# Kernel optimization log

Hardware: AMD Instinct MI355X
Metric: run time of the kernel (lower is better)

The kernel has to match this reference:

```python
import jax, jax.numpy as jnp
import numpy as np

C_IN = 96          # spectral bands
D2 = 2 * C_IN      # d = 192 (inner dim)
D4 = 4 * D2        # 768 (4-directional scan channels)
N = 16             # SSM state size
DR = 6             # delta_rank = ceil(96/16)
B, H, W = 2, 96, 96  # H,W not in {8,16,32,64} -> s=1 path


def setup_inputs() -> dict:
    key = jax.random.key(0)
    ks = jax.random.split(key, 8)
    g = lambda k, shape, s: jax.random.normal(k, shape, jnp.float32) * s
    return {
        "x": jax.random.normal(ks[0], (B, C_IN, H, W), jnp.float32),
        "W_in": g(ks[1], (C_IN, 2 * D2), 0.05),          # in_proj (in,out)
        "b_in": jnp.zeros((2 * D2,), jnp.float32),
        "w_dw": g(ks[2], (D2, 1, 3, 3), 0.1),            # depthwise conv OIHW
        "b_dw": jnp.zeros((D2,), jnp.float32),
        "A_log": jnp.log(jnp.tile(jnp.arange(1.0, N + 1.0, dtype=jnp.float32), (D4, 1))),
        "Dp": jnp.ones((D4,), jnp.float32),
        "W_x": g(ks[3], (D4, DR + 2 * N), 0.05),         # x_proj, no bias
        "W_delta": g(ks[4], (DR, D4), 0.1),
        "b_delta": g(ks[5], (D4,), 0.1),
        "ln_g": jnp.ones((D2,), jnp.float32),
        "ln_b": jnp.zeros((D2,), jnp.float32),
        "W_out": g(ks[6], (D2, C_IN), 0.05),             # out_proj, no bias
    }


def _selective_scan(u, delta, A, Bm, Cm, Dv):
    # u, delta: [b,L,d4]; Bm, Cm: [b,L,n]; A: [d4,n]; Dv: [d4]
    b, L, d4 = u.shape
    n = A.shape[1]

    def step(h, inps):
        u_t, dt, B_t, C_t = inps                      # [b,d4],[b,d4],[b,n],[b,n]
        dA = jnp.exp(dt[:, :, None] * A)              # [b,d4,n]
        h = dA * h + (dt * u_t)[:, :, None] * B_t[:, None, :]
        y = jnp.einsum('bdn,bn->bd', h, C_t) + Dv * u_t
        return h, y

    h0 = jnp.zeros((b, d4, n), u.dtype)
    xs = (jnp.swapaxes(u, 0, 1), jnp.swapaxes(delta, 0, 1),
          jnp.swapaxes(Bm, 0, 1), jnp.swapaxes(Cm, 0, 1))
    _, ys = jax.lax.scan(step, h0, xs)                # ys: [L,b,d4]
    return jnp.swapaxes(ys, 0, 1)                     # [b,L,d4]


def reference(x, W_in, b_in, w_dw, b_dw, A_log, Dp, W_x, W_delta, b_delta, ln_g, ln_b, W_out):
    b, c, Hh, Ww = x.shape                            # s = 1 (H not in {8,16,32,64})
    d = W_in.shape[1] // 2
    # in_proj on channel-last, chunk into x / gate z
    xz = jnp.einsum('bchw,ce->bhwe', x, W_in) + b_in  # [b,h,w,2d]
    xx, z = jnp.split(xz, 2, axis=-1)
    # depthwise conv + silu
    xc = jnp.transpose(xx, (0, 3, 1, 2))              # [b,d,h,w]
    xc = jax.lax.conv_general_dilated(
        xc, w_dw, (1, 1), 'SAME', feature_group_count=d,
        dimension_numbers=('NCHW', 'OIHW', 'NCHW')) + b_dw[None, :, None, None]
    xc = jax.nn.silu(xc)
    # 4 directional flattenings (with s=1: x1==x2 row-major, x3==x4 reversed)
    L = Hh * Ww
    flat = xc.reshape(b, d, L)
    flipped = xc[:, :, ::-1, ::-1].reshape(b, d, L)
    xl = jnp.swapaxes(jnp.concatenate([flat, flat, flipped, flipped], axis=1), 1, 2)  # [b,L,4d]
    # SSM parameterization
    A = -jnp.exp(A_log)                               # [4d,n]
    x_dbl = xl @ W_x                                  # [b,L,dr+2n]
    dr, n = W_delta.shape[0], A.shape[1]
    dt_r = x_dbl[..., :dr]
    Bm = x_dbl[..., dr:dr + n]
    Cm = x_dbl[..., dr + n:]
    delta = jax.nn.softplus(dt_r @ W_delta + b_delta)  # [b,L,4d]
    y = _selective_scan(xl, delta, A, Bm, Cm, Dp)      # [b,L,4d]
    # merge 4 directions back to spatial
    y = jnp.transpose(y.reshape(b, L, 4, d), (0, 2, 3, 1))  # [b,4,d,L]
    y1 = y[:, 0].reshape(b, d, Hh, Ww)
    y2 = y[:, 1].reshape(b, d, Hh, Ww)
    y3 = y[:, 2].reshape(b, d, Hh, Ww)[:, :, ::-1, ::-1]
    y4 = y[:, 3].reshape(b, d, Hh, Ww)[:, :, ::-1, ::-1]
    yh = jnp.transpose(y1 + y2 + y3 + y4, (0, 2, 3, 1))  # [b,h,w,d]
    # LayerNorm over d
    mu = yh.mean(-1, keepdims=True)
    var = ((yh - mu) ** 2).mean(-1, keepdims=True)
    yn = (yh - mu) * jax.lax.rsqrt(var + 1e-5) * ln_g + ln_b
    out = (yn * jax.nn.silu(z)) @ W_out               # [b,h,w,c]
    return jnp.transpose(out, (0, 3, 1, 2))           # [b,c,h,w]
```

## Files before the change

### kernel.cpp

```cpp
#include <hip/hip_runtime.h>
#include <hip/hip_bf16.h>
#include <math.h>

#define CIN 96
#define D2 192
#define D4 768
#define LL 9216
#define NN 16
#define NCH 192
#define CLEN 48

typedef float v2f __attribute__((ext_vector_type(2)));

#define SZ_Y4SLOT (2u*2u*9216u*192u)
#define SZ_BL    (2u*9216u*192u)
#define SZ_XDBL  (2u*9216u*38u)
#define SZ_S     (2u*4u*192u*192u)
#define SZ_H     (2u*4u*192u*192u*16u)
#define F_Y4     0u
#define F_XX     0u
#define F_ZS     (F_Y4 + SZ_Y4SLOT)
#define F_XT     (F_ZS + SZ_BL)
#define F_XD0    (F_XT + SZ_BL)
#define F_XD1    (F_XD0 + SZ_XDBL)
#define F_XD2    (F_XD1 + SZ_XDBL)
#define F_XD3    (F_XD2 + SZ_XDBL)
#define F_SBUF   (F_XD3 + SZ_XDBL)
#define F_HBUF   (F_SBUF + SZ_S)
#define F_WCOMB  (F_HBUF + SZ_H)

__device__ __forceinline__ float silu_f(float z) {
    return z / (1.0f + __expf(-z));
}

__device__ __forceinline__ void pow_pairs(float e1, v2f p[8]) {
    float e2 = e1 * e1;
    v2f p01; p01.x = e1; p01.y = e2;
    v2f e2v; e2v.x = e2; e2v.y = e2;
    v2f e4v = e2v * e2v;
    v2f e8v = e4v * e4v;
    p[0] = p01;
    p[1] = p01 * e2v;
    p[2] = p01 * e4v;
    p[3] = p[1] * e4v;
    p[4] = p01 * e8v;
    p[5] = p[1] * e8v;
    p[6] = p[2] * e8v;
    p[7] = p[3] * e8v;
}

__global__ __launch_bounds__(256) void k0_foldw(
    const float* __restrict__ Wx, float* __restrict__ wcomb)
{
    int i = blockIdx.x * 256 + threadIdx.x;
    if (i >= 192 * 80) return;
    int d = i / 80, j = i % 80;
    float v = 0.f;
    if (j < 38) v = Wx[d * 38 + j] + Wx[(d + 192) * 38 + j];
    else if (j >= 40 && j < 78) {
        int jj = j - 40;
        v = Wx[(d + 384) * 38 + jj] + Wx[(d + 576) * 38 + jj];
    }
    wcomb[i] = v;
}

__global__ __launch_bounds__(256) void k1_inproj(
    const float* __restrict__ x, const float* __restrict__ Win,
    const float* __restrict__ bin, float* __restrict__ xx, float* __restrict__ zs)
{
    __shared__ float xs[96][68];
    __shared__ float wsm[96][68];
    int tid = threadIdx.x;
    int gl0 = blockIdx.x * 64;
    int b = gl0 / LL;
    int l0 = gl0 % LL;

    for (int i = tid; i < 96 * 64; i += 256) {
        int k = i >> 6, li = i & 63;
        xs[k][li] = x[(size_t)(b * 96 + k) * LL + l0 + li];
    }
    int lg = tid >> 4;
    int eg = tid & 15;
    for (int ech = 0; ech < 384; ech += 64) {
        __syncthreads();
        for (int i = tid; i < 96 * 64; i += 256) {
            int k = i >> 6, e = i & 63;
            wsm[k][e] = Win[k * 384 + ech + e];
        }
        __syncthreads();
        v2f acc2[4][2];
#pragma unroll
        for (int i = 0; i < 4; i++)
#pragma unroll
            for (int p = 0; p < 2; p++) { acc2[i][p].x = 0.f; acc2[i][p].y = 0.f; }
        for (int k = 0; k < 96; k++) {
            float4 xv = *(const float4*)&xs[k][lg * 4];
            float4 wv = *(const float4*)&wsm[k][eg * 4];
            v2f w0; w0.x = wv.x; w0.y = wv.y;
            v2f w1; w1.x = wv.z; w1.y = wv.w;
            float xa[4] = {xv.x, xv.y, xv.z, xv.w};
#pragma unroll
            for (int i = 0; i < 4; i++) {
                v2f xsp; xsp.x = xa[i]; xsp.y = xa[i];
                acc2[i][0] += xsp * w0;
                acc2[i][1] += xsp * w1;
            }
        }
        int e0 = ech + eg * 4;
        if (e0 < 192) {
#pragma unroll
            for (int j = 0; j < 4; j++) {
                int e = e0 + j;
                float bb = bin[e];
                float4 v = {acc2[0][j >> 1][j & 1] + bb, acc2[1][j >> 1][j & 1] + bb,
                            acc2[2][j >> 1][j & 1] + bb, acc2[3][j >> 1][j & 1] + bb};
                *(float4*)&xx[(size_t)(b * 192 + e) * LL + l0 + lg * 4] = v;
            }
        } else {
#pragma unroll
            for (int i = 0; i < 4; i++) {
                int l = l0 + lg * 4 + i;
                float4 v;
                v.x = silu_f(acc2[i][0][0] + bin[e0 + 0]);
                v.y = silu_f(acc2[i][0][1] + bin[e0 + 1]);
                v.z = silu_f(acc2[i][1][0] + bin[e0 + 2]);
                v.w = silu_f(acc2[i][1][1] + bin[e0 + 3]);
                *(float4*)&zs[((size_t)b * LL + l) * 192 + (e0 - 192)] = v;
            }
        }
    }
}

__global__ __launch_bounds__(192) void k2_conv(
    const float* __restrict__ xx, const float* __restrict__ wdw,
    const float* __restrict__ bdw, float* __restrict__ xt)
{
    __shared__ float tile[32][97];
    __shared__ float wsm[32][9];
    __shared__ float bs[32];
    int tid = threadIdx.x;
    int bid = blockIdx.x;
    int h = bid % 96;
    int r = bid / 96;
    int dg = r % 6;
    int b = r / 6;

    for (int i = tid; i < 288; i += 192) wsm[i / 9][i % 9] = wdw[(dg * 32 + i / 9) * 9 + (i % 9)];
    if (tid < 32) bs[tid] = bdw[dg * 32 + tid];
    __syncthreads();

    int w = tid % 96;
    int dhalf = tid / 96;
    for (int p = 0; p < 16; p++) {
        int dsub = 2 * p + dhalf;
        const float* base = xx + (size_t)(b * 192 + dg * 32 + dsub) * LL;
        float acc = bs[dsub];
#pragma unroll
        for (int kh = 0; kh < 3; kh++) {
            int hh = h + kh - 1;
            if (hh < 0 || hh >= 96) continue;
            const float* row = base + hh * 96;
#pragma unroll
            for (int kw = 0; kw < 3; kw++) {
                int ww = w + kw - 1;
                if (ww < 0 || ww >= 96) continue;
                acc += row[ww] * wsm[dsub][kh * 3 + kw];
            }
        }
        tile[dsub][w] = silu_f(acc);
    }
    __syncthreads();
    for (int i = tid; i < 768; i += 192) {
        int q = i & 7, ls = i >> 3;
        float4 v = {tile[q * 4 + 0][ls], tile[q * 4 + 1][ls], tile[q * 4 + 2][ls], tile[q * 4 + 3][ls]};
        *(float4*)&xt[((size_t)b * LL + h * 96 + ls) * 192 + dg * 32 + q * 4] = v;
    }
}

__global__ __launch_bounds__(320) void k3_xdbl(
    const float* __restrict__ xt, const float* __restrict__ wcomb,
    float* __restrict__ xa0, float* __restrict__ xa1,
    float* __restrict__ xb0, float* __restrict__ xb1)
{
    __shared__ float xs[16][68];
    __shared__ float wsh[16][80];
    int tid = threadIdx.x;
    int bid = blockIdx.x;
    int kh = bid & 1;
    int rt = (bid >> 1) % 144;
    int b = bid / 288;
    int r0 = rt * 64;
    int k0 = kh * 96;
    float* __restrict__ xa = kh ? xa1 : xa0;
    float* __restrict__ xb = kh ? xb1 : xb0;

    int rg = tid / 20;
    int cg = tid % 20;
    v2f acc[4][2];
#pragma unroll
    for (int i = 0; i < 4; i++)
#pragma unroll
        for (int p = 0; p < 2; p++) { acc[i][p].x = 0.f; acc[i][p].y = 0.f; }

    for (int kc = 0; kc < 96; kc += 16) {
        __syncthreads();
        if (tid < 256) {
            int row = tid >> 2, dq = tid & 3;
            float4 v = *(const float4*)&xt[((size_t)b * LL + r0 + row) * 192 + k0 + kc + dq * 4];
            xs[dq * 4 + 0][row] = v.x;
            xs[dq * 4 + 1][row] = v.y;
            xs[dq * 4 + 2][row] = v.z;
            xs[dq * 4 + 3][row] = v.w;
        }
        for (int i = tid; i < 16 * 80; i += 320) {
            int d = i / 80, j = i - d * 80;
            wsh[d][j] = wcomb[(k0 + kc + d) * 80 + j];
        }
        __syncthreads();
#pragma unroll
        for (int d = 0; d < 16; d++) {
            float4 xv = *(const float4*)&xs[d][rg * 4];
            float4 wv = *(const float4*)&wsh[d][cg * 4];
            v2f w01; w01.x = wv.x; w01.y = wv.y;
            v2f w23; w23.x = wv.z; w23.y = wv.w;
            float xr[4] = {xv.x, xv.y, xv.z, xv.w};
#pragma unroll
            for (int i = 0; i < 4; i++) {
                v2f xi; xi.x = xr[i]; xi.y = xr[i];
                acc[i][0] += xi * w01;
                acc[i][1] += xi * w23;
            }
        }
    }
    int c0 = cg * 4;
#pragma unroll
    for (int i = 0; i < 4; i++) {
        int la = r0 + rg * 4 + i;
#pragma unroll
        for (int j = 0; j < 4; j++) {
            int col = c0 + j;
            float v = acc[i][j >> 1][j & 1];
            if (col < 38) {
                xa[((size_t)b * LL + la) * 38 + col] = v;
            } else if (col >= 40 && col < 78) {
                int lb = LL - 1 - la;
                xb[((size_t)b * LL + lb) * 38 + (col - 40)] = v;
            }
        }
    }
}

__global__ __launch_bounds__(192, 4) void k4_pass1(
    const float* __restrict__ xt,
    const float* __restrict__ xa0, const float* __restrict__ xa1,
    const float* __restrict__ xb0, const float* __restrict__ xb1,
    const float* __restrict__ Wd, const float* __restrict__ bdl,
    const float* __restrict__ Alog,
    float* __restrict__ Sbuf, float* __restrict__ Hbuf)
{
    __shared__ float Bt[CLEN][16];
    __shared__ float Dt[CLEN][6];
    int tid = threadIdx.x;
    int bid = blockIdx.x;
    int k = bid % NCH;
    int r = bid / NCH;
    int dir = r & 3;
    int b = r >> 2;
    int l0 = k * CLEN;
    for (int i = tid; i < CLEN * 16; i += 192) {
        int t = i >> 4, n = i & 15;
        size_t rb = ((size_t)b * LL + l0 + t) * 38 + 6 + n;
        Bt[t][n] = (xa0[rb] + xa1[rb]) + (xb0[rb] + xb1[rb]);
    }
    for (int i = tid; i < CLEN * 6; i += 192) {
        int t = i / 6, rr = i - 6 * t;
        size_t rb = ((size_t)b * LL + l0 + t) * 38 + rr;
        Dt[t][rr] = (xa0[rb] + xa1[rb]) + (xb0[rb] + xb1[rb]);
    }
    __syncthreads();
    int c = tid;
    int d4 = dir * 192 + c;
    float a0 = -__expf(Alog[d4 * 16]);
    bool fast = true;
    for (int n = 1; n < 16; n++) {
        float an = -__expf(Alog[d4 * 16 + n]);
        float tgt = (n + 1) * a0;
        fast = fast && (fabsf(an - tgt) <= 1e-5f * fabsf(tgt));
    }
    float wd[6];
#pragma unroll
    for (int rr = 0; rr < 6; rr++) wd[rr] = Wd[rr * 768 + d4];
    float bde = bdl[d4];
    float S = 0.f;
    const float* xtp = xt + (size_t)b * LL * 192 + c;
    int bd = b * 4 + dir;
    size_t base = (((size_t)bd * NCH + k) * 192 + c) * 16;
    if (fast) {
        v2f h2[8];
#pragma unroll
        for (int n = 0; n < 8; n++) { h2[n].x = 0.f; h2[n].y = 0.f; }
        for (int t = 0; t < CLEN; t++) {
            float s = bde;
#pragma unroll
            for (int rr = 0; rr < 6; rr++) s += Dt[t][rr] * wd[rr];
            float dt = (s > 20.f) ? s : __logf(1.f + __expf(s));
            S += dt;
            int lp = (dir < 2) ? (l0 + t) : (LL - 1 - (l0 + t));
            float u = xtp[(size_t)lp * 192];
            float du = dt * u;
            float4 q0 = *(const float4*)&Bt[t][0];
            float4 q1 = *(const float4*)&Bt[t][4];
            float4 q2 = *(const float4*)&Bt[t][8];
            float4 q3 = *(const float4*)&Bt[t][12];
            v2f B2[8];
            B2[0].x = q0.x; B2[0].y = q0.y; B2[1].x = q0.z; B2[1].y = q0.w;
            B2[2].x = q1.x; B2[2].y = q1.y; B2[3].x = q1.z; B2[3].y = q1.w;
            B2[4].x = q2.x; B2[4].y = q2.y; B2[5].x = q2.z; B2[5].y = q2.w;
            B2[6].x = q3.x; B2[6].y = q3.y; B2[7].x = q3.z; B2[7].y = q3.w;
            v2f p2[8];
            pow_pairs(__expf(dt * a0), p2);
            v2f du2; du2.x = du; du2.y = du;
#pragma unroll
            for (int n = 0; n < 8; n++) h2[n] = p2[n] * h2[n] + du2 * B2[n];
        }
        v2f* hb = (v2f*)&Hbuf[base];
#pragma unroll
        for (int n = 0; n < 8; n++) hb[n] = h2[n];
    } else {
        float h[16];
#pragma unroll
        for (int n = 0; n < 16; n++) h[n] = 0.f;
        for (int t = 0; t < CLEN; t++) {
            float s = bde;
#pragma unroll
            for (int rr = 0; rr < 6; rr++) s += Dt[t][rr] * wd[rr];
            float dt = (s > 20.f) ? s : __logf(1.f + __expf(s));
            S += dt;
            int lp = (dir < 2) ? (l0 + t) : (LL - 1 - (l0 + t));
            float u = xtp[(size_t)lp * 192];
            float du = dt * u;
#pragma unroll
            for (int n = 0; n < 16; n++) {
                float e = __expf(dt * (-__expf(Alog[d4 * 16 + n])));
                h[n] = e * h[n] + du * Bt[t][n];
            }
        }
#pragma unroll
        for (int n = 0; n < 16; n++) Hbuf[base + n] = h[n];
    }
    Sbuf[((size_t)bd * NCH + k) * 192 + c] = S;
}

__global__ __launch_bounds__(256) void k4_pass2(
    const float* __restrict__ Sbuf, const float* __restrict__ Alog,
    float* __restrict__ Hbuf)
{
    int lane = blockIdx.x * 256 + threadIdx.x;
    int bd = lane / 3072;
    int cn = lane % 3072;
    int c = cn >> 4, n = cn & 15;
    int dir = bd & 3;
    float an = -__expf(Alog[(dir * 192 + c) * 16 + n]);
    float h = 0.f;
#pragma unroll 8
    for (int k = 0; k < NCH; k++) {
        size_t sidx = ((size_t)bd * NCH + k) * 192 + c;
        float S = Sbuf[sidx];
        size_t idx = sidx * 16 + n;
        float hl = Hbuf[idx];
        float P = __expf(an * S);
        Hbuf[idx] = h;
        h = P * h + hl;
    }
}

__global__ __launch_bounds__(192, 4) void k4_pass3(
    const float* __restrict__ xt,
    const float* __restrict__ xa0, const float* __restrict__ xa1,
    const float* __restrict__ xb0, const float* __restrict__ xb1,
    const float* __restrict__ Wd, const float* __restrict__ bdl,
    const float* __restrict__ Alog, const float* __restrict__ Dp,
    const float* __restrict__ Hbuf, __hip_bfloat16* __restrict__ y4)
{
    __shared__ float Bt[CLEN][16];
    __shared__ float Ct[CLEN][16];
    __shared__ float Dt[CLEN][6];
    int tid = threadIdx.x;
    int bid = blockIdx.x;
    int k = bid % NCH;
    int r = bid / NCH;
    int dir = r & 3;
    int b = r >> 2;
    int l0 = k * CLEN;
    for (int i = tid; i < CLEN * 16; i += 192) {
        int t = i >> 4, n = i & 15;
        size_t rb = ((size_t)b * LL + l0 + t) * 38;
        size_t r1 = rb + 6 + n, r2 = rb + 22 + n;
        Bt[t][n] = (xa0[r1] + xa1[r1]) + (xb0[r1] + xb1[r1]);
        Ct[t][n] = (xa0[r2] + xa1[r2]) + (xb0[r2] + xb1[r2]);
    }
    for (int i = tid; i < CLEN * 6; i += 192) {
        int t = i / 6, rr = i - 6 * t;
        size_t rb = ((size_t)b * LL + l0 + t) * 38 + rr;
        Dt[t][rr] = (xa0[rb] + xa1[rb]) + (xb0[rb] + xb1[rb]);
    }
    __syncthreads();
    int c = tid;
    int d4 = dir * 192 + c;
    float a0 = -__expf(Alog[d4 * 16]);
    bool fast = true;
    for (int n = 1; n < 16; n++) {
        float an = -__expf(Alog[d4 * 16 + n]);
        float tgt = (n + 1) * a0;
        fast = fast && (fabsf(an - tgt) <= 1e-5f * fabsf(tgt));
    }
    float wd[6];
#pragma unroll
    for (int rr = 0; rr < 6; rr++) wd[rr] = Wd[rr * 768 + d4];
    float bde = bdl[d4];
    float Dv = Dp[d4];
    int bd = b * 4 + dir;
    size_t base = (((size_t)bd * NCH + k) * 192 + c) * 16;
    const float* xtp = xt + (size_t)b * LL * 192 + c;
    __hip_bfloat16* yp = y4 + (size_t)bd * LL * 192 + c;
    if (fast) {
        v2f h2[8];
        const v2f* hb = (const v2f*)&Hbuf[base];
#pragma unroll
        for (int n = 0; n < 8; n++) h2[n] = hb[n];
        for (int t = 0; t < CLEN; t++) {
            float s = bde;
#pragma unroll
            for (int rr = 0; rr < 6; rr++) s += Dt[t][rr] * wd[rr];
            float dt = (s > 20.f) ? s : __logf(1.f + __expf(s));
            int lp = (dir < 2) ? (l0 + t) : (LL - 1 - (l0 + t));
            float u = xtp[(size_t)lp * 192];
            float du = dt * u;
            float4 q0 = *(const float4*)&Bt[t][0];
            float4 q1 = *(const float4*)&Bt[t][4];
            float4 q2 = *(const float4*)&Bt[t][8];
            float4 q3 = *(const float4*)&Bt[t][12];
            v2f B2[8];
            B2[0].x = q0.x; B2[0].y = q0.y; B2[1].x = q0.z; B2[1].y = q0.w;
            B2[2].x = q1.x; B2[2].y = q1.y; B2[3].x = q1.z; B2[3].y = q1.w;
            B2[4].x = q2.x; B2[4].y = q2.y; B2[5].x = q2.z; B2[5].y = q2.w;
            B2[6].x = q3.x; B2[6].y = q3.y; B2[7].x = q3.z; B2[7].y = q3.w;
            float4 r0 = *(const float4*)&Ct[t][0];
            float4 r1 = *(const float4*)&Ct[t][4];
            float4 r2 = *(const float4*)&Ct[t][8];
            float4 r3 = *(const float4*)&Ct[t][12];
            v2f C2[8];
            C2[0].x = r0.x; C2[0].y = r0.y; C2[1].x = r0.z; C2[1].y = r0.w;
            C2[2].x = r1.x; C2[2].y = r1.y; C2[3].x = r1.z; C2[3].y = r1.w;
            C2[4].x = r2.x; C2[4].y = r2.y; C2[5].x = r2.z; C2[5].y = r2.w;
            C2[6].x = r3.x; C2[6].y = r3.y; C2[7].x = r3.z; C2[7].y = r3.w;
            v2f p2[8];
            pow_pairs(__expf(dt * a0), p2);
            v2f du2; du2.x = du; du2.y = du;
            v2f ya; ya.x = 0.f; ya.y = 0.f;
            v2f yb; yb.x = 0.f; yb.y = 0.f;
#pragma unroll
            for (int n = 0; n < 8; n += 2) {
                h2[n] = p2[n] * h2[n] + du2 * B2[n];
                ya += h2[n] * C2[n];
                h2[n + 1] = p2[n + 1] * h2[n + 1] + du2 * B2[n + 1];
                yb += h2[n + 1] * C2[n + 1];
            }
            float yv = (ya.x + ya.y) + (yb.x + yb.y) + Dv * u;
            yp[(size_t)lp * 192] = __float2bfloat16(yv);
        }
    } else {
        float h[16];
#pragma unroll
        for (int n = 0; n < 16; n++) h[n] = Hbuf[base + n];
        for (int t = 0; t < CLEN; t++) {
            float s = bde;
#pragma unroll
            for (int rr = 0; rr < 6; rr++) s += Dt[t][rr] * wd[rr];
            float dt = (s > 20.f) ? s : __logf(1.f + __expf(s));
            int lp = (dir < 2) ? (l0 + t) : (LL - 1 - (l0 + t));
            float u = xtp[(size_t)lp * 192];
            float du = dt * u;
            float yv = Dv * u;
#pragma unroll
            for (int n = 0; n < 16; n++) {
                float e = __expf(dt * (-__expf(Alog[d4 * 16 + n])));
                h[n] = e * h[n] + du * Bt[t][n];
                yv += h[n] * Ct[t][n];
            }
            yp[(size_t)lp * 192] = __float2bfloat16(yv);
        }
    }
}

__global__ __launch_bounds__(256) void k5_out(
    const __hip_bfloat16* __restrict__ y4, const float* __restrict__ zs,
    const float* __restrict__ lng, const float* __restrict__ lnb,
    const float* __restrict__ Wout, float* __restrict__ out)
{
    __shared__ float acts[64][194];
    __shared__ float wsh[32][100];
    int tid = threadIdx.x;
    int wv = tid >> 6;
    int lane = tid & 63;
    int gl0 = blockIdx.x * 64;
    int b = gl0 / LL;
    int l0 = gl0 % LL;
    const size_t ds = (size_t)LL * 192;

    for (int i = 0; i < 16; i++) {
        int rrow = wv * 16 + i;
        int l = l0 + rrow;
        float yv[3], zv[3];
        float s1 = 0.f, s2 = 0.f;
#pragma unroll
        for (int kk = 0; kk < 3; kk++) {
            int c = lane + kk * 64;
            size_t off = ((size_t)(b * 4) * LL + l) * 192 + c;
            float y = __bfloat162float(y4[off]) + __bfloat162float(y4[off + ds])
                    + __bfloat162float(y4[off + 2 * ds]) + __bfloat162float(y4[off + 3 * ds]);
            yv[kk] = y;
            zv[kk] = zs[((size_t)b * LL + l) * 192 + c];
            s1 += y; s2 += y * y;
        }
#pragma unroll
        for (int o = 32; o; o >>= 1) {
            s1 += __shfl_xor(s1, o, 64);
            s2 += __shfl_xor(s2, o, 64);
        }
        float mean = s1 * (1.f / 192.f);
        float var = s2 * (1.f / 192.f) - mean * mean;
        float rs = rsqrtf(var + 1e-5f);
#pragma unroll
        for (int kk = 0; kk < 3; kk++) {
            int c = lane + kk * 64;
            float yn = (yv[kk] - mean) * rs * lng[c] + lnb[c];
            acts[rrow][c] = yn * zv[kk];
        }
    }

    int ty = tid >> 4;
    int tx = tid & 15;
    v2f o2[4][3];
#pragma unroll
    for (int i = 0; i < 4; i++)
#pragma unroll
        for (int p = 0; p < 3; p++) { o2[i][p].x = 0.f; o2[i][p].y = 0.f; }

    for (int kc = 0; kc < 192; kc += 32) {
        __syncthreads();
        for (int i = tid; i < 3072; i += 256)
            wsh[i / 96][i % 96] = Wout[(kc + i / 96) * 96 + i % 96];
        __syncthreads();
        for (int kk = 0; kk < 32; kk++) {
            float av[4];
#pragma unroll
            for (int i = 0; i < 4; i++) av[i] = acts[ty * 4 + i][kc + kk];
            const v2f* wp = (const v2f*)&wsh[kk][tx * 6];
            v2f w0 = wp[0], w1 = wp[1], w2 = wp[2];
#pragma unroll
            for (int i = 0; i < 4; i++) {
                v2f sp; sp.x = av[i]; sp.y = av[i];
                o2[i][0] += sp * w0;
                o2[i][1] += sp * w1;
                o2[i][2] += sp * w2;
            }
        }
    }
#pragma unroll
    for (int i = 0; i < 4; i++) {
        int l = l0 + ty * 4 + i;
#pragma unroll
        for (int j = 0; j < 6; j++) {
            int n = tx * 6 + j;
            out[((size_t)(b * 96) + n) * LL + l] = o2[i][j >> 1][j & 1];
        }
    }
}

extern "C" void kernel_launch(void* const* d_in, const int* in_sizes, int n_in,
                              void* d_out, int out_size, void* d_ws, size_t ws_size,
                              hipStream_t stream)
{
    const float* x    = (const float*)d_in[0];
    const float* Win  = (const float*)d_in[1];
    const float* bin  = (const float*)d_in[2];
    const float* wdw  = (const float*)d_in[3];
    const float* bdw  = (const float*)d_in[4];
    const float* Alog = (const float*)d_in[5];
    const float* Dp   = (const float*)d_in[6];
    const float* Wx   = (const float*)d_in[7];
    const float* Wd   = (const float*)d_in[8];
    const float* bdl  = (const float*)d_in[9];
    const float* lng  = (const float*)d_in[10];
    const float* lnb  = (const float*)d_in[11];
    const float* Wout = (const float*)d_in[12];
    float* out = (float*)d_out;

    float* ws    = (float*)d_ws;
    __hip_bfloat16* y4 = (__hip_bfloat16*)(ws + F_Y4);
    float* xx    = ws + F_XX;
    float* zs    = ws + F_ZS;
    float* xt    = ws + F_XT;
    float* xd0   = ws + F_XD0;
    float* xd1   = ws + F_XD1;
    float* xd2   = ws + F_XD2;
    float* xd3   = ws + F_XD3;
    float* Sbuf  = ws + F_SBUF;
    float* Hbuf  = ws + F_HBUF;
    float* wcomb = ws + F_WCOMB;

    k0_foldw<<<60, 256, 0, stream>>>(Wx, wcomb);
    k1_inproj<<<288, 256, 0, stream>>>(x, Win, bin, xx, zs);
    k2_conv<<<1152, 192, 0, stream>>>(xx, wdw, bdw, xt);
    k3_xdbl<<<576, 320, 0, stream>>>(xt, wcomb, xd0, xd1, xd2, xd3);
    k4_pass1<<<1536, 192, 0, stream>>>(xt, xd0, xd1, xd2, xd3, Wd, bdl, Alog, Sbuf, Hbuf);
    k4_pass2<<<96, 256, 0, stream>>>(Sbuf, Alog, Hbuf);
    k4_pass3<<<1536, 192, 0, stream>>>(xt, xd0, xd1, xd2, xd3, Wd, bdl, Alog, Dp, Hbuf, y4);
    k5_out<<<288, 256, 0, stream>>>(y4, zs, lng, lnb, Wout, out);
}
```

Before: 322.5 us.

## Shorten scan chunks, store carry states in bf16, halve output tile rows

Scan chunk length drops from 48 to 32, so pass1 and pass3 launch 2304 blocks instead of 1536 and each block does a shorter sequential recurrence. Chunk-boundary states are now stored in bf16, which cuts the state buffer traffic in all three scan passes. The output kernel moves to 32-row tiles with 16-deep K steps, doubling its grid, and the time loops are unrolled by two. The trade-offs are a longer serial prefix in pass2 (288 steps instead of 192), lower precision on the carried states, and less reuse of Wout per block.

After: 306.7 us. -4.9%, faster.

```diff
diff --git a/kernel.cpp b/kernel.cpp
--- a/kernel.cpp
+++ b/kernel.cpp
@@ -7,16 +7,16 @@
 #define D4 768
 #define LL 9216
 #define NN 16
-#define NCH 192
-#define CLEN 48
+#define NCH 288
+#define CLEN 32
 
 typedef float v2f __attribute__((ext_vector_type(2)));
 
 #define SZ_Y4SLOT (2u*2u*9216u*192u)
 #define SZ_BL    (2u*9216u*192u)
 #define SZ_XDBL  (2u*9216u*38u)
-#define SZ_S     (2u*4u*192u*192u)
-#define SZ_H     (2u*4u*192u*192u*16u)
+#define SZ_S     (2u*4u*288u*192u)
+#define SZ_HSLOT (2u*4u*288u*192u*8u)
 #define F_Y4     0u
 #define F_XX     0u
 #define F_ZS     (F_Y4 + SZ_Y4SLOT)
@@ -27,7 +27,7 @@
 #define F_XD3    (F_XD2 + SZ_XDBL)
 #define F_SBUF   (F_XD3 + SZ_XDBL)
 #define F_HBUF   (F_SBUF + SZ_S)
-#define F_WCOMB  (F_HBUF + SZ_H)
+#define F_WCOMB  (F_HBUF + SZ_HSLOT)
 
 __device__ __forceinline__ float silu_f(float z) {
     return z / (1.0f + __expf(-z));
@@ -256,7 +256,7 @@
     const float* __restrict__ xb0, const float* __restrict__ xb1,
     const float* __restrict__ Wd, const float* __restrict__ bdl,
     const float* __restrict__ Alog,
-    float* __restrict__ Sbuf, float* __restrict__ Hbuf)
+    float* __restrict__ Sbuf, __hip_bfloat16* __restrict__ Hbuf)
 {
     __shared__ float Bt[CLEN][16];
     __shared__ float Dt[CLEN][6];
@@ -299,6 +299,7 @@
         v2f h2[8];
 #pragma unroll
         for (int n = 0; n < 8; n++) { h2[n].x = 0.f; h2[n].y = 0.f; }
+#pragma unroll 2
         for (int t = 0; t < CLEN; t++) {
             float s = bde;
 #pragma unroll
@@ -323,9 +324,12 @@
 #pragma unroll
             for (int n = 0; n < 8; n++) h2[n] = p2[n] * h2[n] + du2 * B2[n];
         }
-        v2f* hb = (v2f*)&Hbuf[base];
-#pragma unroll
-        for (int n = 0; n < 8; n++) hb[n] = h2[n];
+        __hip_bfloat16* hb = Hbuf + base;
+#pragma unroll
+        for (int n = 0; n < 8; n++) {
+            hb[2 * n]     = __float2bfloat16(h2[n].x);
+            hb[2 * n + 1] = __float2bfloat16(h2[n].y);
+        }
     } else {
         float h[16];
 #pragma unroll
@@ -346,14 +350,14 @@
             }
         }
 #pragma unroll
-        for (int n = 0; n < 16; n++) Hbuf[base + n] = h[n];
+        for (int n = 0; n < 16; n++) Hbuf[base + n] = __float2bfloat16(h[n]);
     }
     Sbuf[((size_t)bd * NCH + k) * 192 + c] = S;
 }
 
 __global__ __launch_bounds__(256) void k4_pass2(
     const float* __restrict__ Sbuf, const float* __restrict__ Alog,
-    float* __restrict__ Hbuf)
+    __hip_bfloat16* __restrict__ Hbuf)
 {
     int lane = blockIdx.x * 256 + threadIdx.x;
     int bd = lane / 3072;
@@ -367,9 +371,9 @@
         size_t sidx = ((size_t)bd * NCH + k) * 192 + c;
         float S = Sbuf[sidx];
         size_t idx = sidx * 16 + n;
-        float hl = Hbuf[idx];
+        float hl = __bfloat162float(Hbuf[idx]);
         float P = __expf(an * S);
-        Hbuf[idx] = h;
+        Hbuf[idx] = __float2bfloat16(h);
         h = P * h + hl;
     }
 }
@@ -380,7 +384,7 @@
     const float* __restrict__ xb0, const float* __restrict__ xb1,
     const float* __restrict__ Wd, const float* __restrict__ bdl,
     const float* __restrict__ Alog, const float* __restrict__ Dp,
-    const float* __restrict__ Hbuf, __hip_bfloat16* __restrict__ y4)
+    const __hip_bfloat16* __restrict__ Hbuf, __hip_bfloat16* __restrict__ y4)
 {
     __shared__ float Bt[CLEN][16];
     __shared__ float Ct[CLEN][16];
@@ -425,9 +429,13 @@
     __hip_bfloat16* yp = y4 + (size_t)bd * LL * 192 + c;
     if (fast) {
         v2f h2[8];
-        const v2f* hb = (const v2f*)&Hbuf[base];
-#pragma unroll
-        for (int n = 0; n < 8; n++) h2[n] = hb[n];
+        const __hip_bfloat16* hb = Hbuf + base;
+#pragma unroll
+        for (int n = 0; n < 8; n++) {
+            h2[n].x = __bfloat162float(hb[2 * n]);
+            h2[n].y = __bfloat162float(hb[2 * n + 1]);
+        }
+#pragma unroll 2
         for (int t = 0; t < CLEN; t++) {
             float s = bde;
 #pragma unroll
@@ -472,7 +480,7 @@
     } else {
         float h[16];
 #pragma unroll
-        for (int n = 0; n < 16; n++) h[n] = Hbuf[base + n];
+        for (int n = 0; n < 16; n++) h[n] = __bfloat162float(Hbuf[base + n]);
         for (int t = 0; t < CLEN; t++) {
             float s = bde;
 #pragma unroll
@@ -498,18 +506,18 @@
     const float* __restrict__ lng, const float* __restrict__ lnb,
     const float* __restrict__ Wout, float* __restrict__ out)
 {
-    __shared__ float acts[64][194];
-    __shared__ float wsh[32][100];
+    __shared__ float acts[32][196];
+    __shared__ float wsh[16][100];
     int tid = threadIdx.x;
     int wv = tid >> 6;
     int lane = tid & 63;
-    int gl0 = blockIdx.x * 64;
+    int gl0 = blockIdx.x * 32;
     int b = gl0 / LL;
     int l0 = gl0 % LL;
     const size_t ds = (size_t)LL * 192;
 
-    for (int i = 0; i < 16; i++) {
-        int rrow = wv * 16 + i;
+    for (int i = 0; i < 8; i++) {
+        int rrow = wv * 8 + i;
         int l = l0 + rrow;
         float yv[3], zv[3];
         float s1 = 0.f, s2 = 0.f;
@@ -541,35 +549,34 @@
 
     int ty = tid >> 4;
     int tx = tid & 15;
-    v2f o2[4][3];
-#pragma unroll
-    for (int i = 0; i < 4; i++)
+    v2f o2[2][3];
+#pragma unroll
+    for (int i = 0; i < 2; i++)
 #pragma unroll
         for (int p = 0; p < 3; p++) { o2[i][p].x = 0.f; o2[i][p].y = 0.f; }
 
-    for (int kc = 0; kc < 192; kc += 32) {
+    for (int kc = 0; kc < 192; kc += 16) {
         __syncthreads();
-        for (int i = tid; i < 3072; i += 256)
-            wsh[i / 96][i % 96] = Wout[(kc + i / 96) * 96 + i % 96];
+        for (int i = tid; i < 16 * 96; i += 256) {
+            int d = i / 96, j = i - d * 96;
+            wsh[d][j] = Wout[(kc + d) * 96 + j];
+        }
         __syncthreads();
-        for (int kk = 0; kk < 32; kk++) {
-            float av[4];
-#pragma unroll
-            for (int i = 0; i < 4; i++) av[i] = acts[ty * 4 + i][kc + kk];
+#pragma unroll
+        for (int kk = 0; kk < 16; kk++) {
+            float a0v = acts[ty * 2][kc + kk];
+            float a1v = acts[ty * 2 + 1][kc + kk];
             const v2f* wp = (const v2f*)&wsh[kk][tx * 6];
             v2f w0 = wp[0], w1 = wp[1], w2 = wp[2];
-#pragma unroll
-            for (int i = 0; i < 4; i++) {
-                v2f sp; sp.x = av[i]; sp.y = av[i];
-                o2[i][0] += sp * w0;
-                o2[i][1] += sp * w1;
-                o2[i][2] += sp * w2;
-            }
-        }
-    }
-#pragma unroll
-    for (int i = 0; i < 4; i++) {
-        int l = l0 + ty * 4 + i;
+            v2f s0; s0.x = a0v; s0.y = a0v;
+            v2f s1v; s1v.x = a1v; s1v.y = a1v;
+            o2[0][0] += s0 * w0;  o2[0][1] += s0 * w1;  o2[0][2] += s0 * w2;
+            o2[1][0] += s1v * w0; o2[1][1] += s1v * w1; o2[1][2] += s1v * w2;
+        }
+    }
+#pragma unroll
+    for (int i = 0; i < 2; i++) {
+        int l = l0 + ty * 2 + i;
 #pragma unroll
         for (int j = 0; j < 6; j++) {
             int n = tx * 6 + j;
@@ -607,15 +614,15 @@
     float* xd2   = ws + F_XD2;
     float* xd3   = ws + F_XD3;
     float* Sbuf  = ws + F_SBUF;
-    float* Hbuf  = ws + F_HBUF;
+    __hip_bfloat16* Hbuf = (__hip_bfloat16*)(ws + F_HBUF);
     float* wcomb = ws + F_WCOMB;
 
     k0_foldw<<<60, 256, 0, stream>>>(Wx, wcomb);
     k1_inproj<<<288, 256, 0, stream>>>(x, Win, bin, xx, zs);
     k2_conv<<<1152, 192, 0, stream>>>(xx, wdw, bdw, xt);
     k3_xdbl<<<576, 320, 0, stream>>>(xt, wcomb, xd0, xd1, xd2, xd3);
-    k4_pass1<<<1536, 192, 0, stream>>>(xt, xd0, xd1, xd2, xd3, Wd, bdl, Alog, Sbuf, Hbuf);
+    k4_pass1<<<2304, 192, 0, stream>>>(xt, xd0, xd1, xd2, xd3, Wd, bdl, Alog, Sbuf, Hbuf);
     k4_pass2<<<96, 256, 0, stream>>>(Sbuf, Alog, Hbuf);
-    k4_pass3<<<1536, 192, 0, stream>>>(xt, xd0, xd1, xd2, xd3, Wd, bdl, Alog, Dp, Hbuf, y4);
-    k5_out<<<288, 256, 0, stream>>>(y4, zs, lng, lnb, Wout, out);
-}
+    k4_pass3<<<2304, 192, 0, stream>>>(xt, xd0, xd1, xd2, xd3, Wd, bdl, Alog, Dp, Hbuf, y4);
+    k5_out<<<576, 256, 0, stream>>>(y4, zs, lng, lnb, Wout, out);
+}
```
